# Kernel optimization log

Measured on AMD Instinct MI355X. Metric: run time of the kernel, lower is better.

The kernel has to match this reference:

```python
import jax, jax.numpy as jnp
import numpy as np

N_NODES = 1536
IN_FEATURES = 1433
N_HIDDEN = 64      # total across 8 heads -> 8 per head
N_HEADS = 8
N_CLASSES = 7
NEG_SLOPE = 0.2    # LeakyReLU slope in GATv2 layer


def setup_inputs() -> dict:
    key = jax.random.key(0)
    k_x, k_adj, k_w1, k_a1, k_w2, k_a2 = jax.random.split(key, 6)
    x = jax.random.normal(k_x, (N_NODES, IN_FEATURES), dtype=jnp.float32)
    adj = jax.random.uniform(k_adj, (N_NODES, N_NODES)) < 0.01
    adj = adj | jnp.eye(N_NODES, dtype=bool)
    adj_mat = adj[:, :, None]  # [n, n, 1]
    # layer 1 (share_weights=True -> one linear for l and r), attn vector shared across heads
    s1 = 1.0 / np.sqrt(IN_FEATURES)
    W1 = jax.random.uniform(k_w1, (IN_FEATURES, N_HIDDEN), minval=-s1, maxval=s1, dtype=jnp.float32)
    a1 = jax.random.uniform(k_a1, (N_HIDDEN // N_HEADS,), minval=-1.0, maxval=1.0, dtype=jnp.float32)
    # layer 2: 1 head, n_classes features, is_concat=False (mean over the single head)
    s2 = 1.0 / np.sqrt(N_HIDDEN)
    W2 = jax.random.uniform(k_w2, (N_HIDDEN, N_CLASSES), minval=-s2, maxval=s2, dtype=jnp.float32)
    a2 = jax.random.uniform(k_a2, (N_CLASSES,), minval=-1.0, maxval=1.0, dtype=jnp.float32)
    return {"x": x, "adj_mat": adj_mat, "W1": W1, "a1": a1, "W2": W2, "a2": a2}


def _gatv2_layer(h, adj, W, a, n_heads, is_concat):
    n = h.shape[0]
    g = (h @ W).reshape(n, n_heads, -1)              # shared weights: g_l == g_r == g
    # pairwise scores: e[i,j,h] = a . leaky_relu(g[j] + g[i])  (symmetric since weights shared)
    s = jax.nn.leaky_relu(g[:, None] + g[None, :], NEG_SLOPE)   # [n, n, heads, f]
    e = jnp.einsum('ijhf,f->ijh', s, a)                          # [n, n, heads]
    e = jnp.where(adj, e, -jnp.inf)                              # adj broadcasts [n,n,1]
    att = jax.nn.softmax(e, axis=1)                              # softmax over source nodes j
    out = jnp.einsum('ijh,jhf->ihf', att, g)                     # [n, heads, f]
    if is_concat:
        return out.reshape(n, -1)
    return out.mean(axis=1)


def reference(x, adj_mat, W1, a1, W2, a2):
    # dropout layers are identity in eval mode
    h = _gatv2_layer(x, adj_mat, W1, a1, N_HEADS, True)   # [n, n_hidden]
    h = jax.nn.elu(h)
    return _gatv2_layer(h, adj_mat, W2, a2, 1, False)     # [n, n_classes]
```

## Files before the change

### kernel.cpp

```cpp
#include <hip/hip_runtime.h>

#define N_NODES 1536
#define IN_F    1433
#define HID     64
#define NH      8
#define HF      8
#define NC      7
#define MAXN    64
#define GST     66
#define G1_BLOCKS 384
#define ROWS    4
#define XS_STRIDE 1440

__device__ __forceinline__ float waveAllMax(float v) {
#pragma unroll
    for (int o = 32; o > 0; o >>= 1) v = fmaxf(v, __shfl_xor(v, o, 64));
    return v;
}
__device__ __forceinline__ float waveAllSum(float v) {
#pragma unroll
    for (int o = 32; o > 0; o >>= 1) v += __shfl_xor(v, o, 64);
    return v;
}

__global__ __launch_bounds__(256) void k_front(const float* __restrict__ x,
                                               const float* __restrict__ W1,
                                               const unsigned int* __restrict__ adj,
                                               float* __restrict__ g1,
                                               int* __restrict__ cnt,
                                               int* __restrict__ nbr) {
    __shared__ float xs[ROWS * XS_STRIDE];
    __shared__ float red[4 * 256];
    __shared__ int lc;
    const int t = threadIdx.x;

    if (blockIdx.x < G1_BLOCKS) {
        const int i0 = blockIdx.x * ROWS;
        for (int r = 0; r < ROWS; ++r) {
            const float* xr = x + (size_t)(i0 + r) * IN_F;
            for (int k = t; k < XS_STRIDE; k += 256)
                xs[r * XS_STRIDE + k] = (k < IN_F) ? xr[k] : 0.f;
        }
        __syncthreads();
        const int j = t & 63, q = t >> 6;
        float acc[ROWS] = {0.f, 0.f, 0.f, 0.f};
        const int k0 = q * 360;
        for (int kb = k0; kb < k0 + 360; kb += 4) {
            float w[4];
#pragma unroll
            for (int u = 0; u < 4; ++u) {
                int k = kb + u;
                int kc = (k < IN_F) ? k : (IN_F - 1);
                w[u] = W1[(size_t)kc * HID + j];
            }
#pragma unroll
            for (int r = 0; r < ROWS; ++r) {
                float4 xv = *(const float4*)(xs + r * XS_STRIDE + kb);
                acc[r] += xv.x * w[0] + xv.y * w[1] + xv.z * w[2] + xv.w * w[3];
            }
        }
#pragma unroll
        for (int r = 0; r < ROWS; ++r) red[q * 256 + r * 64 + j] = acc[r];
        __syncthreads();
        float s = red[0 * 256 + t] + red[1 * 256 + t] + red[2 * 256 + t] + red[3 * 256 + t];
        g1[(size_t)(i0 + (t >> 6)) * HID + (t & 63)] = s;
    } else {
        const int i = blockIdx.x - G1_BLOCKS;
        if (t == 0) lc = 0;
        __syncthreads();
        const unsigned int* row = adj + (size_t)i * N_NODES;
        for (int j = t; j < N_NODES; j += 256) {
            if (row[j] != 0u) {
                int p = atomicAdd(&lc, 1);
                if (p < MAXN) nbr[i * MAXN + p] = j;
            }
        }
        __syncthreads();
        if (t == 0) {
            int n = (lc > MAXN) ? MAXN : lc;
            if (n == 0) { nbr[i * MAXN] = i; n = 1; }
            cnt[i] = n;
        }
    }
}

__global__ __launch_bounds__(128) void k_attn1(const float* __restrict__ g1,
                                               const int* __restrict__ cnt,
                                               const int* __restrict__ nbr,
                                               const float* __restrict__ a1,
                                               const float* __restrict__ W2,
                                               float* __restrict__ g2) {
    __shared__ float gis[HID];
    __shared__ float gj[MAXN * GST];
    __shared__ float es[NH * GST];
    __shared__ float hrow[HID];
    const int i = blockIdx.x, tid = threadIdx.x;
    const int t = tid & 63, w = tid >> 6;
    const int n = cnt[i];

    if (tid < HID) gis[tid] = g1[(size_t)i * HID + tid];
    const int jn = nbr[i * MAXN + t];

    for (int l0 = 4 * w; l0 < n; l0 += 8) {
        float v[4];
#pragma unroll
        for (int u = 0; u < 4; ++u) {
            int l = l0 + u;
            int lc = (l < n) ? l : (n - 1);
            int j = __shfl(jn, lc, 64);
            v[u] = g1[(size_t)j * HID + t];
        }
#pragma unroll
        for (int u = 0; u < 4; ++u)
            if (l0 + u < n) gj[(l0 + u) * GST + t] = v[u];
    }
    __syncthreads();

    float av[HF];
#pragma unroll
    for (int f = 0; f < HF; ++f) av[f] = a1[f];

    float sc[4];
    if (t < n) {
#pragma unroll
        for (int hh = 0; hh < 4; ++hh) {
            const int h = 4 * w + hh;
            float s = 0.f;
#pragma unroll
            for (int f = 0; f < HF; ++f) {
                float v = gis[h * HF + f] + gj[t * GST + h * HF + f];
                v = (v >= 0.f) ? v : 0.2f * v;
                s += av[f] * v;
            }
            sc[hh] = s;
        }
    } else {
#pragma unroll
        for (int hh = 0; hh < 4; ++hh) sc[hh] = -INFINITY;
    }

#pragma unroll
    for (int hh = 0; hh < 4; ++hh) {
        const int h = 4 * w + hh;
        float m = waveAllMax(sc[hh]);
        float p = (t < n) ? __expf(sc[hh] - m) : 0.f;
        float S = waveAllSum(p);
        es[h * GST + t] = p / S;
    }

    const int c = 32 * w + (t & 31);
    const int h = c >> 3;
    float acc = 0.f;
    for (int l = (t >> 5); l < n; l += 2)
        acc += es[h * GST + l] * gj[l * GST + c];
    acc += __shfl_xor(acc, 32, 64);
    float hv = (acc > 0.f) ? acc : (__expf(acc) - 1.f);
    if (t < 32) hrow[c] = hv;
    __syncthreads();

    const float hvt = hrow[t];
#pragma unroll
    for (int cc = 0; cc < 4; ++cc) {
        const int cG = 4 * w + cc;
        if (cG < NC) {
            float v = hvt * W2[t * NC + cG];
            v = waveAllSum(v);
            if (t == 0) g2[(size_t)i * 8 + cG] = v;
        }
    }
}

__global__ __launch_bounds__(64) void k_back(const float* __restrict__ g2,
                                             const float* __restrict__ a2,
                                             const int* __restrict__ cnt,
                                             const int* __restrict__ nbr,
                                             float* __restrict__ out) {
    __shared__ float g2s[MAXN * 8];
    const int i = blockIdx.x, t = threadIdx.x;
    const int n = cnt[i];
    const int jn = nbr[i * MAXN + t];
    const int j = (t < n) ? jn : i;

    float4 lo = *(const float4*)(g2 + (size_t)j * 8);
    float4 hi = *(const float4*)(g2 + (size_t)j * 8 + 4);
    float4 slo = *(const float4*)(g2 + (size_t)i * 8);
    float4 shi = *(const float4*)(g2 + (size_t)i * 8 + 4);
    *(float4*)(g2s + t * 8) = lo;
    *(float4*)(g2s + t * 8 + 4) = hi;
    __syncthreads();

    const float self[NC] = {slo.x, slo.y, slo.z, slo.w, shi.x, shi.y, shi.z};

    float scv;
    if (t < n) {
        float s = 0.f;
#pragma unroll
        for (int c = 0; c < NC; ++c) {
            float v = self[c] + g2s[t * 8 + c];
            v = (v >= 0.f) ? v : 0.2f * v;
            s += a2[c] * v;
        }
        scv = s;
    } else scv = -INFINITY;

    float m = waveAllMax(scv);
    float p = (t < n) ? __expf(scv - m) : 0.f;
    float S = waveAllSum(p);

#pragma unroll
    for (int c = 0; c < NC; ++c) {
        float v = (t < n) ? p * g2s[t * 8 + c] : 0.f;
        float s = waveAllSum(v);
        if (t == c) out[(size_t)i * NC + c] = s / S;
    }
}

extern "C" void kernel_launch(void* const* d_in, const int* in_sizes, int n_in,
                              void* d_out, int out_size, void* d_ws, size_t ws_size,
                              hipStream_t stream) {
    (void)out_size; (void)ws_size;
    const void* px = nullptr; const void* padj = nullptr;
    const void* pW1 = nullptr; const void* pa1 = nullptr;
    const void* pW2 = nullptr; const void* pa2 = nullptr;
    for (int i = 0; i < n_in; ++i) {
        switch (in_sizes[i]) {
            case N_NODES * IN_F:    px   = d_in[i]; break;
            case N_NODES * N_NODES: padj = d_in[i]; break;
            case IN_F * HID:        pW1  = d_in[i]; break;
            case HF:                pa1  = d_in[i]; break;
            case HID * NC:          pW2  = d_in[i]; break;
            case NC:                pa2  = d_in[i]; break;
            default: break;
        }
    }
    if (!px && n_in > 0)   px   = d_in[0];
    if (!padj && n_in > 1) padj = d_in[1];
    if (!pW1 && n_in > 2)  pW1  = d_in[2];
    if (!pa1 && n_in > 3)  pa1  = d_in[3];
    if (!pW2 && n_in > 4)  pW2  = d_in[4];
    if (!pa2 && n_in > 5)  pa2  = d_in[5];

    char* w = (char*)d_ws;
    size_t off = 0;
    auto carve = [&](size_t bytes) -> char* {
        off = (off + 255) & ~(size_t)255;
        char* p = w + off; off += bytes; return p;
    };
    int*   cnt = (int*)  carve((size_t)N_NODES * 4);
    int*   nbr = (int*)  carve((size_t)N_NODES * MAXN * 4);
    float* g1  = (float*)carve((size_t)N_NODES * HID * 4);
    float* g2  = (float*)carve((size_t)N_NODES * 8 * 4);

    float* outp = (float*)d_out;

    k_front<<<G1_BLOCKS + N_NODES, 256, 0, stream>>>((const float*)px, (const float*)pW1,
                                                     (const unsigned int*)padj, g1, cnt, nbr);
    k_attn1<<<N_NODES, 128, 0, stream>>>(g1, cnt, nbr, (const float*)pa1,
                                         (const float*)pW2, g2);
    k_back<<<N_NODES, 64, 0, stream>>>(g2, (const float*)pa2, cnt, nbr, outp);
}
```

Measured before the change: 110.4 us.

## Retile x@W1 GEMM with 4-column register tiles and 16-way K split

Changes the thread mapping of the first-layer x@W1 GEMM. Each thread now owns 4 output columns across 4 rows and loads W1 as float4, with K split 16 ways (92 each) instead of 4 ways (360 each). The result is more FMAs per W1 and shared-memory load and shorter per-thread K loops, at the cost of a larger 16-way reduction in shared memory and a padded x staging buffer.

```diff
diff --git a/kernel.cpp b/kernel.cpp
--- a/kernel.cpp
+++ b/kernel.cpp
@@ -10,7 +10,9 @@
 #define GST     66
 #define G1_BLOCKS 384
 #define ROWS    4
-#define XS_STRIDE 1440
+#define KQ      92
+#define XS2     1472
+#define RED_ST  260
 
 __device__ __forceinline__ float waveAllMax(float v) {
 #pragma unroll
@@ -29,8 +31,8 @@
                                                float* __restrict__ g1,
                                                int* __restrict__ cnt,
                                                int* __restrict__ nbr) {
-    __shared__ float xs[ROWS * XS_STRIDE];
-    __shared__ float red[4 * 256];
+    __shared__ float xs[ROWS * XS2];
+    __shared__ float red[16 * RED_ST];
     __shared__ int lc;
     const int t = threadIdx.x;
 
@@ -38,31 +40,49 @@
         const int i0 = blockIdx.x * ROWS;
         for (int r = 0; r < ROWS; ++r) {
             const float* xr = x + (size_t)(i0 + r) * IN_F;
-            for (int k = t; k < XS_STRIDE; k += 256)
-                xs[r * XS_STRIDE + k] = (k < IN_F) ? xr[k] : 0.f;
-        }
-        __syncthreads();
-        const int j = t & 63, q = t >> 6;
-        float acc[ROWS] = {0.f, 0.f, 0.f, 0.f};
-        const int k0 = q * 360;
-        for (int kb = k0; kb < k0 + 360; kb += 4) {
-            float w[4];
+            for (int k = t; k < XS2; k += 256)
+                xs[r * XS2 + k] = (k < IN_F) ? xr[k] : 0.f;
+        }
+        __syncthreads();
+
+        const int tc = t & 15;
+        const int tq = t >> 4;
+        const int k0 = tq * KQ;
+        float acc[ROWS][4];
+#pragma unroll
+        for (int r = 0; r < ROWS; ++r)
+#pragma unroll
+            for (int cc = 0; cc < 4; ++cc) acc[r][cc] = 0.f;
+
+        for (int kb = k0; kb < k0 + KQ; kb += 4) {
+            float wv[4][4];
 #pragma unroll
             for (int u = 0; u < 4; ++u) {
-                int k = kb + u;
-                int kc = (k < IN_F) ? k : (IN_F - 1);
-                w[u] = W1[(size_t)kc * HID + j];
+                int kc = kb + u;
+                if (kc > IN_F - 1) kc = IN_F - 1;
+                float4 wq = *(const float4*)(W1 + (size_t)kc * HID + tc * 4);
+                wv[u][0] = wq.x; wv[u][1] = wq.y; wv[u][2] = wq.z; wv[u][3] = wq.w;
             }
 #pragma unroll
             for (int r = 0; r < ROWS; ++r) {
-                float4 xv = *(const float4*)(xs + r * XS_STRIDE + kb);
-                acc[r] += xv.x * w[0] + xv.y * w[1] + xv.z * w[2] + xv.w * w[3];
-            }
-        }
-#pragma unroll
-        for (int r = 0; r < ROWS; ++r) red[q * 256 + r * 64 + j] = acc[r];
-        __syncthreads();
-        float s = red[0 * 256 + t] + red[1 * 256 + t] + red[2 * 256 + t] + red[3 * 256 + t];
+                float4 xq = *(const float4*)(xs + r * XS2 + kb);
+                float xr4[4] = {xq.x, xq.y, xq.z, xq.w};
+#pragma unroll
+                for (int u = 0; u < 4; ++u)
+#pragma unroll
+                    for (int cc = 0; cc < 4; ++cc)
+                        acc[r][cc] += xr4[u] * wv[u][cc];
+            }
+        }
+#pragma unroll
+        for (int r = 0; r < ROWS; ++r)
+#pragma unroll
+            for (int cc = 0; cc < 4; ++cc)
+                red[tq * RED_ST + r * 64 + tc * 4 + cc] = acc[r][cc];
+        __syncthreads();
+        float s = 0.f;
+#pragma unroll
+        for (int q = 0; q < 16; ++q) s += red[q * RED_ST + t];
         g1[(size_t)(i0 + (t >> 6)) * HID + (t & 63)] = s;
     } else {
         const int i = blockIdx.x - G1_BLOCKS;
```

Result: faster. 102.2 us (-7.5%).
